# Performance work log

Measured on AMD Instinct MI355X. Metric: run time of the kernel, lower is better.

## Reference

```python
import jax, jax.numpy as jnp
import numpy as np

N, D_HID, D_PROJ = 10000, 256, 256
TAU = 0.5


def setup_inputs() -> dict:
    key = jax.random.key(0)
    ks = jax.random.split(key, 7)
    s = 1.0 / np.sqrt(D_HID)
    return {
        "z1": jax.random.normal(ks[0], (N, D_HID), jnp.float32),
        "z2": jax.random.normal(ks[1], (N, D_HID), jnp.float32),
        "z3": jax.random.normal(ks[2], (N, D_HID), jnp.float32),
        "W1": jax.random.normal(ks[3], (D_PROJ, D_HID), jnp.float32) * s,
        "b1": jnp.zeros((D_PROJ,), jnp.float32),
        "W2": jax.random.normal(ks[4], (D_HID, D_PROJ), jnp.float32) * s,
        "b2": jnp.zeros((D_HID,), jnp.float32),
    }


def _projection(z, W1, b1, W2, b2):
    h = jax.nn.elu(z @ W1.T + b1)
    return h @ W2.T + b2


def _normalize(z, eps=1e-12):
    n = jnp.linalg.norm(z, axis=1, keepdims=True)
    return z / jnp.maximum(n, eps)


def _semi_loss(z1, z2, z3, tau):
    # exp of three NxN cosine-similarity matrices / tau
    intra = jnp.exp(z1 @ z1.T / tau)
    inter = jnp.exp(z1 @ z2.T / tau)
    neg = jnp.exp(z1 @ z3.T / tau)
    denom = (intra.sum(1) + inter.sum(1) + neg.sum(1)
             - jnp.diag(intra) - jnp.diag(inter) - jnp.diag(neg))
    return -jnp.log(jnp.diag(inter) / denom)


def reference(z1, z2, z3, W1, b1, W2, b2):
    p1 = _normalize(_projection(z1, W1, b1, W2, b2))
    p2 = _normalize(_projection(z2, W1, b1, W2, b2))
    p3 = _normalize(_projection(z3, W1, b1, W2, b2))
    l1 = _semi_loss(p1, p2, p3, TAU)
    l2 = _semi_loss(p2, p1, p3, TAU)
    return ((l1 + l2) * 0.5).mean()
```

## Files before the change

### kernel.cpp

```cpp
#include <hip/hip_runtime.h>
#include <hip/hip_bf16.h>
#include <hip/hip_fp8.h>
#include <math.h>

#define AS1 __attribute__((address_space(1)))
#define AS3 __attribute__((address_space(3)))

typedef __bf16 bf16x8 __attribute__((ext_vector_type(8)));
typedef __bf16 bf16x4 __attribute__((ext_vector_type(4)));
typedef float  f32x4  __attribute__((ext_vector_type(4)));
typedef long   longx2 __attribute__((ext_vector_type(2)));

static constexpr int   N_ROWS   = 10000;
static constexpr int   D        = 256;

static constexpr int   T        = 79;
static constexpr int   NP       = T * 128;
static constexpr float PADF     = 112.0f;
static constexpr int   SPR     = 10;
static constexpr int   BPJ     = T * SPR;
static constexpr int   NWGG    = 5 * BPJ;

static constexpr int   PT       = 79;

__device__ __forceinline__ void tile_gemm_128(
    const __bf16* __restrict__ Abase, const __bf16* __restrict__ Bbase,
    char* ldsA, char* ldsB, int tid, f32x4 acc[4][4])
{
  const int l      = tid & 63;
  const int wr     = (tid >> 7) & 1;
  const int wc     = (tid >> 6) & 1;
  const int srow   = tid >> 3;
  const int schunk = tid & 7;
  const int lrow   = l & 15;
  const int lk     = l >> 4;

  for (int kt = 0; kt < 4; ++kt) {
    __syncthreads();
    const int kbase = kt * 64;
#pragma unroll
    for (int rr = 0; rr < 4; ++rr) {
      const int row = rr * 32 + srow;
      const int lc  = schunk ^ (row & 7);
      const __bf16* ga = Abase + (size_t)row * D + kbase + lc * 8;
      const __bf16* gb = Bbase + (size_t)row * D + kbase + lc * 8;
      __builtin_amdgcn_global_load_lds((const AS1 void*)ga,
          (AS3 void*)(ldsA + rr * 4096 + tid * 16), 16, 0, 0);
      __builtin_amdgcn_global_load_lds((const AS1 void*)gb,
          (AS3 void*)(ldsB + rr * 4096 + tid * 16), 16, 0, 0);
    }
    __syncthreads();
#pragma unroll
    for (int ks = 0; ks < 2; ++ks) {
      bf16x8 af[4], bfr[4];
#pragma unroll
      for (int m = 0; m < 4; ++m) {
        const int row = wr * 64 + m * 16 + lrow;
        const int off = row * 128 + ((ks * 64 + lk * 16) ^ ((row & 7) << 4));
        af[m] = *(const bf16x8*)(ldsA + off);
      }
#pragma unroll
      for (int n = 0; n < 4; ++n) {
        const int row = wc * 64 + n * 16 + lrow;
        const int off = row * 128 + ((ks * 64 + lk * 16) ^ ((row & 7) << 4));
        bfr[n] = *(const bf16x8*)(ldsB + off);
      }
#pragma unroll
      for (int m = 0; m < 4; ++m)
#pragma unroll
        for (int n = 0; n < 4; ++n)
          acc[m][n] = __builtin_amdgcn_mfma_f32_16x16x32_bf16(
              af[m], bfr[n], acc[m][n], 0, 0, 0);
    }
  }
}

__global__ __launch_bounds__(256, 3) void gram_kernel(
    const unsigned char* __restrict__ p1, const unsigned char* __restrict__ p2,
    const unsigned char* __restrict__ p3, float* __restrict__ S)
{
  const int bid = blockIdx.x;
  const int job = bid / BPJ;
  const int t0  = bid % BPJ;
  const int r   = t0 / SPR;
  const int s   = t0 % SPR;
  int cstart = s * 8;
  const int cend = min(cstart + 8, T);

  const unsigned char *P, *Q;
  float *Srow, *Scol;
  bool sym = false;
  if (job == 0)      { P = p1; Q = p2; Srow = S + 1 * NP; Scol = S + 3 * NP; }
  else if (job == 1) { P = p1; Q = p3; Srow = S + 2 * NP; Scol = nullptr; }
  else if (job == 2) { P = p2; Q = p3; Srow = S + 5 * NP; Scol = nullptr; }
  else if (job == 3) { P = p1; Q = p1; Srow = S + 0 * NP; Scol = S + 0 * NP;
                       sym = true; cstart = max(cstart, r); }
  else               { P = p2; Q = p2; Srow = S + 4 * NP; Scol = S + 4 * NP;
                       sym = true; cstart = max(cstart, r); }
  const int len = cend - cstart;
  if (len <= 0) return;
  const int nsteps = len * 4;

  __shared__ __align__(16) char lds[49152];
  char* ldsB = lds + 32768;

  const int tid  = threadIdx.x;
  const int l    = tid & 63;
  const int wave = tid >> 6;
  const int wr   = wave >> 1;
  const int wc   = wave & 1;
  const int lrow = l & 15;
  const int lk   = l >> 4;

  int offA[4][4];
#pragma unroll
  for (int m = 0; m < 4; ++m) {
    const int row = wr * 64 + m * 16 + lrow;
    const int swz = (row >> 1) & 7;
#pragma unroll
    for (int kt = 0; kt < 4; ++kt)
      offA[kt][m] = row * 256 + (((kt * 4 + lk) ^ swz) << 4);
  }
  int offB[4];
#pragma unroll
  for (int n = 0; n < 4; ++n) {
    const int row = wc * 64 + n * 16 + lrow;
    offB[n] = row * 64 + ((lk ^ ((row >> 1) & 3)) << 4);
  }

  const unsigned char* Abase = P + (size_t)r * 128 * 256;
#pragma unroll
  for (int j = 0; j < 8; ++j) {
    const int p = tid + j * 256;
    const int row = p >> 4, pc = p & 15;
    __builtin_amdgcn_global_load_lds(
        (const AS1 void*)(Abase + (size_t)row * 256 +
                          ((pc ^ ((row >> 1) & 7)) << 4)),
        (AS3 void*)(lds + p * 16), 16, 0, 0);
  }

  auto stageB = [&](int buf, int i) {
    const int c  = cstart + (i >> 2);
    const int kb = (i & 3) * 64;
    const unsigned char* B0 = Q + (size_t)c * 128 * 256 + kb;
    char* lb = ldsB + buf * 8192;
#pragma unroll
    for (int j = 0; j < 2; ++j) {
      const int p = tid + j * 256;
      const int row = p >> 2, pc = p & 3;
      __builtin_amdgcn_global_load_lds(
          (const AS1 void*)(B0 + (size_t)row * 256 +
                            ((pc ^ ((row >> 1) & 3)) << 4)),
          (AS3 void*)(lb + p * 16), 16, 0, 0);
    }
  };
  stageB(0, 0);

  f32x4 rsum[4];
#pragma unroll
  for (int m = 0; m < 4; ++m)
#pragma unroll
    for (int q = 0; q < 4; ++q) rsum[m][q] = 0.f;

  for (int tt = 0; tt < len; ++tt) {
    f32x4 acc[4][4];
#pragma unroll
    for (int m = 0; m < 4; ++m)
#pragma unroll
      for (int n = 0; n < 4; ++n)
#pragma unroll
        for (int q = 0; q < 4; ++q) acc[m][n][q] = 0.f;

#pragma unroll
    for (int kt = 0; kt < 4; ++kt) {
      const int i = tt * 4 + kt;
      __syncthreads();
      if (i + 1 < nsteps) stageB((i + 1) & 1, i + 1);
      const char* lb = ldsB + (i & 1) * 8192;
      longx2 af[4], bfr[4];
#pragma unroll
      for (int m = 0; m < 4; ++m)
        af[m] = *(const longx2*)(lds + offA[kt][m]);
#pragma unroll
      for (int n = 0; n < 4; ++n)
        bfr[n] = *(const longx2*)(lb + offB[n]);
#pragma unroll
      for (int m = 0; m < 4; ++m)
#pragma unroll
        for (int n = 0; n < 4; ++n)
          acc[m][n] = __builtin_amdgcn_mfma_f32_16x16x32_fp8_fp8(
              af[m][0], bfr[n][0], acc[m][n], 0, 0, 0);
#pragma unroll
      for (int m = 0; m < 4; ++m)
#pragma unroll
        for (int n = 0; n < 4; ++n)
          acc[m][n] = __builtin_amdgcn_mfma_f32_16x16x32_fp8_fp8(
              af[m][1], bfr[n][1], acc[m][n], 0, 0, 0);
    }

    const int c = cstart + tt;
#pragma unroll
    for (int m = 0; m < 4; ++m)
#pragma unroll
      for (int n = 0; n < 4; ++n)
#pragma unroll
        for (int q = 0; q < 4; ++q)
          acc[m][n][q] = __expf(acc[m][n][q]);

#pragma unroll
    for (int m = 0; m < 4; ++m)
      rsum[m] += acc[m][0] + acc[m][1] + acc[m][2] + acc[m][3];

    const bool docol = Scol && (!sym || c > r);
    if (docol) {
#pragma unroll
      for (int n = 0; n < 4; ++n) {
        float sc = 0.f;
#pragma unroll
        for (int m = 0; m < 4; ++m)
#pragma unroll
          for (int q = 0; q < 4; ++q) sc += acc[m][n][q];
        sc += __shfl_xor(sc, 16, 64);
        sc += __shfl_xor(sc, 32, 64);
        if (l < 16) atomicAdd(&Scol[c * 128 + wc * 64 + n * 16 + l], sc);
      }
    }
  }

#pragma unroll
  for (int m = 0; m < 4; ++m) {
#pragma unroll
    for (int mask = 1; mask < 16; mask <<= 1)
#pragma unroll
      for (int q = 0; q < 4; ++q)
        rsum[m][q] += __shfl_xor(rsum[m][q], mask, 64);
    if ((l & 15) == 0) {
      const int grow = r * 128 + wr * 64 + m * 16 + lk * 4;
#pragma unroll
      for (int q = 0; q < 4; ++q) atomicAdd(&Srow[grow + q], rsum[m][q]);
    }
  }
}

template <int MODE>
__global__ __launch_bounds__(256, 2) void proj_kernel(
    const __bf16* __restrict__ A, const __bf16* __restrict__ B,
    const float* __restrict__ bias, void* __restrict__ out,
    size_t strideA, size_t strideOut)
{
  const int r = blockIdx.x, c = blockIdx.y;
  const size_t zo = (size_t)blockIdx.z;
  A += zo * strideA;
  __shared__ __align__(16) char lds[32768];
  f32x4 acc[4][4];
#pragma unroll
  for (int m = 0; m < 4; ++m)
#pragma unroll
    for (int n = 0; n < 4; ++n)
#pragma unroll
      for (int q = 0; q < 4; ++q) acc[m][n][q] = 0.f;

  tile_gemm_128(A + (size_t)r * 128 * D, B + (size_t)c * 128 * D,
                lds, lds + 16384, threadIdx.x, acc);

  const int tid = threadIdx.x, l = tid & 63;
  const int wr = (tid >> 7) & 1, wc = (tid >> 6) & 1;
#pragma unroll
  for (int n = 0; n < 4; ++n) {
    const int gcol = c * 128 + wc * 64 + n * 16 + (l & 15);
    const float bn = bias[gcol];
#pragma unroll
    for (int m = 0; m < 4; ++m) {
#pragma unroll
      for (int q = 0; q < 4; ++q) {
        const int grow = r * 128 + wr * 64 + m * 16 + (l >> 4) * 4 + q;
        float v = acc[m][n][q] + bn;
        if (MODE == 0) {
          float o = v > 0.f ? v : (__expf(v) - 1.f);
          ((__bf16*)out)[zo * strideOut + (size_t)grow * D + gcol] = (__bf16)o;
        } else {
          ((float*)out)[zo * strideOut + (size_t)grow * D + gcol] = v;
        }
      }
    }
  }
}

__global__ void cast_kernel(const float* __restrict__ src,
                            __bf16* __restrict__ dst, int n)
{
  int idx = (blockIdx.x * blockDim.x + threadIdx.x) * 4;
  const int stride = gridDim.x * blockDim.x * 4;
  for (; idx < n; idx += stride) {
    const float4 v = *(const float4*)(src + idx);
    bf16x4 o;
    o[0] = (__bf16)v.x; o[1] = (__bf16)v.y;
    o[2] = (__bf16)v.z; o[3] = (__bf16)v.w;
    *(bf16x4*)(dst + idx) = o;
  }
}

__global__ void cast3_kernel(const float* __restrict__ z0,
                             const float* __restrict__ z1,
                             const float* __restrict__ z2,
                             __bf16* __restrict__ dst, size_t strideElems)
{
  const int n = N_ROWS * D;
  int idx = (blockIdx.x * blockDim.x + threadIdx.x) * 4;
  const int stride = gridDim.x * blockDim.x * 4;
  for (; idx < 3 * n; idx += stride) {
    const int m = idx / n, e = idx - m * n;
    const float* src = (m == 0) ? z0 : (m == 1) ? z1 : z2;
    const float4 v = *(const float4*)(src + e);
    bf16x4 o;
    o[0] = (__bf16)v.x; o[1] = (__bf16)v.y;
    o[2] = (__bf16)v.z; o[3] = (__bf16)v.w;
    *(bf16x4*)(dst + m * strideElems + e) = o;
  }
}

__global__ void norm_kernel(const float* __restrict__ praw,
                            __bf16* __restrict__ p,
                            unsigned char* __restrict__ pf)
{
  const size_t mo = (size_t)blockIdx.y * NP * D;
  const int row = blockIdx.x * 4 + (threadIdx.x >> 6);
  const int l = threadIdx.x & 63;
  const size_t base = mo + (size_t)row * D + l * 4;
  if (row < N_ROWS) {
    const float4 v = *(const float4*)(praw + base);
    float ss = v.x * v.x + v.y * v.y + v.z * v.z + v.w * v.w;
#pragma unroll
    for (int mask = 1; mask < 64; mask <<= 1) ss += __shfl_xor(ss, mask, 64);
    const float inv = 1.0f / fmaxf(sqrtf(ss), 1e-12f);
    const float f0 = v.x * inv, f1 = v.y * inv, f2 = v.z * inv, f3 = v.w * inv;
    bf16x4 o;
    o[0] = (__bf16)f0; o[1] = (__bf16)f1; o[2] = (__bf16)f2; o[3] = (__bf16)f3;
    *(bf16x4*)(p + base) = o;
    const float SC = 1.41421356237f;
    const unsigned int b0 = __hip_fp8_e4m3(f0 * SC).__x;
    const unsigned int b1 = __hip_fp8_e4m3(f1 * SC).__x;
    const unsigned int b2 = __hip_fp8_e4m3(f2 * SC).__x;
    const unsigned int b3 = __hip_fp8_e4m3(f3 * SC).__x;
    *(unsigned int*)(pf + base) = b0 | (b1 << 8) | (b2 << 16) | (b3 << 24);
  } else {
    bf16x4 o;
    o[0] = o[1] = o[2] = o[3] = (__bf16)0.0f;
    *(bf16x4*)(p + base) = o;
    *(unsigned int*)(pf + base) = 0u;
  }
}

__global__ void diag_kernel(const __bf16* __restrict__ p1,
                            const __bf16* __restrict__ p2,
                            const __bf16* __restrict__ p3,
                            float* __restrict__ dg)
{
  const int row = blockIdx.x * 4 + (threadIdx.x >> 6);
  const int l = threadIdx.x & 63;
  if (row >= N_ROWS) return;
  const size_t base = (size_t)row * D + l * 4;
  const bf16x4 a = *(const bf16x4*)(p1 + base);
  const bf16x4 b = *(const bf16x4*)(p2 + base);
  const bf16x4 e = *(const bf16x4*)(p3 + base);
  float d11 = 0, d22 = 0, d12 = 0, d13 = 0, d23 = 0;
#pragma unroll
  for (int q = 0; q < 4; ++q) {
    const float fa = (float)a[q], fb = (float)b[q], fe = (float)e[q];
    d11 += fa * fa; d22 += fb * fb; d12 += fa * fb;
    d13 += fa * fe; d23 += fb * fe;
  }
#pragma unroll
  for (int mask = 1; mask < 64; mask <<= 1) {
    d11 += __shfl_xor(d11, mask, 64);
    d22 += __shfl_xor(d22, mask, 64);
    d12 += __shfl_xor(d12, mask, 64);
    d13 += __shfl_xor(d13, mask, 64);
    d23 += __shfl_xor(d23, mask, 64);
  }
  if (l == 0) {
    dg[0 * NP + row] = __expf(d11 * 2.0f);
    dg[1 * NP + row] = __expf(d22 * 2.0f);
    dg[2 * NP + row] = __expf(d12 * 2.0f);
    dg[3 * NP + row] = __expf(d13 * 2.0f);
    dg[4 * NP + row] = __expf(d23 * 2.0f);
  }
}

__global__ void loss_kernel(const float* __restrict__ S,
                            const float* __restrict__ dg,
                            float* __restrict__ out)
{
  float local = 0.f;
  for (int i = blockIdx.x * blockDim.x + threadIdx.x; i < N_ROWS;
       i += gridDim.x * blockDim.x) {
    const float s11 = S[0 * NP + i] - PADF;
    const float s12 = S[1 * NP + i] - PADF;
    const float s13 = S[2 * NP + i] - PADF;
    const float s21 = S[3 * NP + i] - PADF;
    const float s22 = S[4 * NP + i] - PADF;
    const float s23 = S[5 * NP + i] - PADF;
    const float d11 = dg[0 * NP + i], d22 = dg[1 * NP + i];
    const float d12 = dg[2 * NP + i], d13 = dg[3 * NP + i];
    const float d23 = dg[4 * NP + i];
    const float den1 = s11 + s12 + s13 - d11 - d12 - d13;
    const float den2 = s22 + s21 + s23 - d22 - d12 - d23;
    local += 0.5f * (__logf(den1) + __logf(den2)) - __logf(d12);
  }
#pragma unroll
  for (int mask = 1; mask < 64; mask <<= 1) local += __shfl_xor(local, mask, 64);
  __shared__ float wsum[4];
  if ((threadIdx.x & 63) == 0) wsum[threadIdx.x >> 6] = local;
  __syncthreads();
  if (threadIdx.x == 0) {
    const float t = wsum[0] + wsum[1] + wsum[2] + wsum[3];
    atomicAdd(out, t * (1.0f / (float)N_ROWS));
  }
}

extern "C" void kernel_launch(void* const* d_in, const int* in_sizes, int n_in,
                              void* d_out, int out_size, void* d_ws,
                              size_t ws_size, hipStream_t stream)
{
  const float* z[3] = {(const float*)d_in[0], (const float*)d_in[1],
                       (const float*)d_in[2]};
  const float* W1 = (const float*)d_in[3];
  const float* b1 = (const float*)d_in[4];
  const float* W2 = (const float*)d_in[5];
  const float* b2 = (const float*)d_in[6];

  char* ws = (char*)d_ws;
  size_t off = 0;
  auto alloc = [&](size_t bytes) -> char* {
    char* p = ws + off;
    off += (bytes + 511) & ~(size_t)511;
    return p;
  };
  const size_t PE = (size_t)NP * D;
  __bf16*        pB3 = (__bf16*)alloc(3 * PE * 2);
  unsigned char* pF3 = (unsigned char*)alloc(3 * PE);
  __bf16* w1b  = (__bf16*)alloc((size_t)D * D * 2);
  __bf16* w2b  = (__bf16*)alloc((size_t)D * D * 2);
  float*  Sv   = (float*) alloc((size_t)6 * NP * 4);
  float*  dg   = (float*) alloc((size_t)5 * NP * 4);

  const size_t common = off;
  const size_t batched_need = common + 3 * ((PE * 2 + 511 & ~511ull) +
                              (PE * 2 + 511 & ~511ull)) + 3 * (PE * 4) + 4096;
  const bool batched = ws_size >= batched_need;

  hipMemsetAsync(Sv, 0, (size_t)6 * NP * 4, stream);
  hipMemsetAsync(d_out, 0, sizeof(float), stream);

  cast_kernel<<<64, 256, 0, stream>>>(W1, w1b, D * D);
  cast_kernel<<<64, 256, 0, stream>>>(W2, w2b, D * D);

  if (batched) {
    __bf16* zb3   = (__bf16*)alloc(3 * PE * 2);
    __bf16* hB3   = (__bf16*)alloc(3 * PE * 2);
    float*  praw3 = (float*) alloc(3 * PE * 4);
    cast3_kernel<<<2048, 256, 0, stream>>>(z[0], z[1], z[2], zb3, PE);
    dim3 g(PT, 2, 3);
    proj_kernel<0><<<g, 256, 0, stream>>>(zb3, w1b, b1, (void*)hB3, PE, PE);
    proj_kernel<1><<<g, 256, 0, stream>>>(hB3, w2b, b2, (void*)praw3, PE, PE);
    dim3 gn(NP / 4, 3);
    norm_kernel<<<gn, 256, 0, stream>>>(praw3, pB3, pF3);
  } else {
    __bf16* zb   = (__bf16*)alloc(PE * 2);
    __bf16* hB   = (__bf16*)alloc(PE * 2);
    float*  praw = (float*) alloc(PE * 4);
    for (int m = 0; m < 3; ++m) {
      cast_kernel<<<2500, 256, 0, stream>>>(z[m], zb, N_ROWS * D);
      dim3 g(PT, 2, 1);
      proj_kernel<0><<<g, 256, 0, stream>>>(zb, w1b, b1, (void*)hB, 0, 0);
      proj_kernel<1><<<g, 256, 0, stream>>>(hB, w2b, b2, (void*)praw, 0, 0);
      dim3 gn(NP / 4, 1);
      norm_kernel<<<gn, 256, 0, stream>>>(praw, pB3 + m * PE, pF3 + m * PE);
    }
  }

  gram_kernel<<<NWGG, 256, 0, stream>>>(pF3, pF3 + PE, pF3 + 2 * PE, Sv);
  diag_kernel<<<2500, 256, 0, stream>>>(pB3, pB3 + PE, pB3 + 2 * PE, dg);
  loss_kernel<<<64, 256, 0, stream>>>(Sv, dg, (float*)d_out);
}
```

Measured before the change: 211.3 us.

## Overlap exp epilogue of previous tile with MFMAs of next tile

Double-buffers the gram kernel accumulators so the exponent, row-sum and column-sum work for the previous tile runs interleaved with the matrix-core instructions of the current tile. It also switches to exp2 by folding log2(e) into the fp8 quantization scale. The change is meant to hide the transcendental and reduction epilogue behind MFMA latency. In exchange, register pressure doubles, so occupancy is lowered to two blocks per CU, and the fp8 scale moves closer to the range limit.

```diff
diff --git a/kernel.cpp b/kernel.cpp
--- a/kernel.cpp
+++ b/kernel.cpp
@@ -75,7 +75,7 @@
   }
 }
 
-__global__ __launch_bounds__(256, 3) void gram_kernel(
+__global__ __launch_bounds__(256, 2) void gram_kernel(
     const unsigned char* __restrict__ p1, const unsigned char* __restrict__ p2,
     const unsigned char* __restrict__ p3, float* __restrict__ S)
 {
@@ -162,8 +162,25 @@
 #pragma unroll
     for (int q = 0; q < 4; ++q) rsum[m][q] = 0.f;
 
-  for (int tt = 0; tt < len; ++tt) {
-    f32x4 acc[4][4];
+  auto do_colsum = [&](f32x4 (&a)[4][4], int c) {
+    const bool docol = Scol && (!sym || c > r);
+    if (docol) {
+#pragma unroll
+      for (int n = 0; n < 4; ++n) {
+        float sc = 0.f;
+#pragma unroll
+        for (int m = 0; m < 4; ++m)
+#pragma unroll
+          for (int q = 0; q < 4; ++q) sc += a[m][n][q];
+        sc += __shfl_xor(sc, 16, 64);
+        sc += __shfl_xor(sc, 32, 64);
+        if (l < 16) atomicAdd(&Scol[c * 128 + wc * 64 + n * 16 + l], sc);
+      }
+    }
+  };
+
+  auto run_tile = [&](f32x4 (&acc)[4][4], f32x4 (&prev)[4][4],
+                      int tt, bool do_prev, int prev_c) {
 #pragma unroll
     for (int m = 0; m < 4; ++m)
 #pragma unroll
@@ -196,36 +213,39 @@
         for (int n = 0; n < 4; ++n)
           acc[m][n] = __builtin_amdgcn_mfma_f32_16x16x32_fp8_fp8(
               af[m][1], bfr[n][1], acc[m][n], 0, 0, 0);
-    }
-
-    const int c = cstart + tt;
-#pragma unroll
-    for (int m = 0; m < 4; ++m)
+      if (do_prev) {
+#pragma unroll
+        for (int n = 0; n < 4; ++n)
+#pragma unroll
+          for (int q = 0; q < 4; ++q)
+            prev[kt][n][q] = exp2f(prev[kt][n][q]);
+        rsum[kt] += prev[kt][0] + prev[kt][1] + prev[kt][2] + prev[kt][3];
+        if (kt == 3) do_colsum(prev, prev_c);
+      }
+    }
+  };
+
+  auto final_epilogue = [&](f32x4 (&a)[4][4], int c) {
+#pragma unroll
+    for (int m = 0; m < 4; ++m) {
 #pragma unroll
       for (int n = 0; n < 4; ++n)
 #pragma unroll
         for (int q = 0; q < 4; ++q)
-          acc[m][n][q] = __expf(acc[m][n][q]);
-
-#pragma unroll
-    for (int m = 0; m < 4; ++m)
-      rsum[m] += acc[m][0] + acc[m][1] + acc[m][2] + acc[m][3];
-
-    const bool docol = Scol && (!sym || c > r);
-    if (docol) {
-#pragma unroll
-      for (int n = 0; n < 4; ++n) {
-        float sc = 0.f;
-#pragma unroll
-        for (int m = 0; m < 4; ++m)
-#pragma unroll
-          for (int q = 0; q < 4; ++q) sc += acc[m][n][q];
-        sc += __shfl_xor(sc, 16, 64);
-        sc += __shfl_xor(sc, 32, 64);
-        if (l < 16) atomicAdd(&Scol[c * 128 + wc * 64 + n * 16 + l], sc);
-      }
-    }
-  }
+          a[m][n][q] = exp2f(a[m][n][q]);
+      rsum[m] += a[m][0] + a[m][1] + a[m][2] + a[m][3];
+    }
+    do_colsum(a, c);
+  };
+
+  f32x4 accA[4][4], accB[4][4];
+  for (int tt = 0; tt < len; ++tt) {
+    const int pc = cstart + tt - 1;
+    if ((tt & 1) == 0) run_tile(accA, accB, tt, tt > 0, pc);
+    else               run_tile(accB, accA, tt, true, pc);
+  }
+  if ((len & 1) == 1) final_epilogue(accA, cstart + len - 1);
+  else                final_epilogue(accB, cstart + len - 1);
 
 #pragma unroll
   for (int m = 0; m < 4; ++m) {
@@ -337,7 +357,7 @@
     bf16x4 o;
     o[0] = (__bf16)f0; o[1] = (__bf16)f1; o[2] = (__bf16)f2; o[3] = (__bf16)f3;
     *(bf16x4*)(p + base) = o;
-    const float SC = 1.41421356237f;
+    const float SC = 1.6986436f;
     const unsigned int b0 = __hip_fp8_e4m3(f0 * SC).__x;
     const unsigned int b1 = __hip_fp8_e4m3(f1 * SC).__x;
     const unsigned int b2 = __hip_fp8_e4m3(f2 * SC).__x;
```

New measurement: 327.8 us. 1.55x slower.
